# Kernel tuning notes

Hardware: AMD Instinct MI355X
Metric: run time of the kernel (lower is better)

## Reference

```python
import jax, jax.numpy as jnp
import numpy as np

D_MODEL = 256
D_STATE = 16
D_CONV = 4
EXPAND = 2
D_INNER = EXPAND * D_MODEL          # 512
DT_RANK = (D_MODEL + 15) // 16      # 16
B_SZ = 4
L_SEQ = 2048
EPS = 1e-5


def setup_inputs() -> dict:
    key = jax.random.key(0)
    ks = jax.random.split(key, 10)
    s = 0.02
    return {
        "x": jax.random.normal(ks[0], (B_SZ, L_SEQ, D_MODEL), jnp.float32),
        # Mamba params
        "in_proj_w": jax.random.normal(ks[1], (2 * D_INNER, D_MODEL), jnp.float32) * s,
        "conv_w": jax.random.normal(ks[2], (D_INNER, 1, D_CONV), jnp.float32) * s,  # depthwise
        "conv_b": jnp.zeros((D_INNER,), jnp.float32),
        "x_proj_w": jax.random.normal(ks[3], (DT_RANK + 2 * D_STATE, D_INNER), jnp.float32) * s,
        "dt_proj_w": jax.random.normal(ks[4], (D_INNER, DT_RANK), jnp.float32) * s,
        "dt_proj_b": jax.random.uniform(ks[5], (D_INNER,), jnp.float32, -4.0, -2.0),
        "A_log": jnp.log(jnp.broadcast_to(jnp.arange(1, D_STATE + 1, dtype=jnp.float32), (D_INNER, D_STATE))),
        "Dp": jnp.ones((D_INNER,), jnp.float32),
        "out_proj_w": jax.random.normal(ks[6], (D_MODEL, D_INNER), jnp.float32) * s,
        # LayerNorms
        "ln1_g": jnp.ones((D_MODEL,), jnp.float32), "ln1_b": jnp.zeros((D_MODEL,), jnp.float32),
        "ln2_g": jnp.ones((D_MODEL,), jnp.float32), "ln2_b": jnp.zeros((D_MODEL,), jnp.float32),
        # temp_enhance: Conv1d(d_model, d_model, k=3, pad=1, groups=4) + BatchNorm1d (eval buffers)
        "enh_w": jax.random.normal(ks[7], (D_MODEL, D_MODEL // 4, 3), jnp.float32) * s,
        "enh_b": jnp.zeros((D_MODEL,), jnp.float32),
        "bn_g": jnp.ones((D_MODEL,), jnp.float32), "bn_b": jnp.zeros((D_MODEL,), jnp.float32),
        "bn_mean": jnp.zeros((D_MODEL,), jnp.float32), "bn_var": jnp.ones((D_MODEL,), jnp.float32),
    }


def _layernorm(x, g, b):
    m = x.mean(-1, keepdims=True)
    v = ((x - m) ** 2).mean(-1, keepdims=True)
    return (x - m) * jax.lax.rsqrt(v + EPS) * g + b


def _mamba(x, in_proj_w, conv_w, conv_b, x_proj_w, dt_proj_w, dt_proj_b, A_log, Dp, out_proj_w):
    Bb, L, _ = x.shape
    # input projection -> gate z and conv stream
    xz = x @ in_proj_w.T                       # [B, L, 2*d_inner]
    xin, z = jnp.split(xz, 2, axis=-1)
    # causal depthwise conv over time
    xc = jnp.transpose(xin, (0, 2, 1))         # [B, d_inner, L]
    xc = jax.lax.conv_general_dilated(
        xc, conv_w, (1,), [(D_CONV - 1, 0)],
        dimension_numbers=("NCH", "OIH", "NCH"), feature_group_count=D_INNER)
    xc = xc + conv_b[None, :, None]
    xin = jax.nn.silu(jnp.transpose(xc, (0, 2, 1)))   # [B, L, d_inner]
    # input-dependent dt, B, C
    x_dbl = xin @ x_proj_w.T                   # [B, L, dt_rank + 2*d_state]
    dt, Bm, Cm = jnp.split(x_dbl, [DT_RANK, DT_RANK + D_STATE], axis=-1)
    dt = jax.nn.softplus(dt @ dt_proj_w.T + dt_proj_b)   # [B, L, d_inner]
    A = -jnp.exp(A_log)                         # [d_inner, d_state]
    dA = jnp.exp(dt[..., None] * A)             # [B, L, d_inner, d_state]
    dBx = dt[..., None] * Bm[:, :, None, :] * xin[..., None]
    # selective scan: h_t = dA_t * h_{t-1} + dBx_t ; y_t = <h_t, C_t>
    def step(h, inputs):
        a, bx, c = inputs
        h = a * h + bx                          # [B, d_inner, d_state]
        y = jnp.einsum("bds,bs->bd", h, c)
        return h, y
    h0 = jnp.zeros((Bb, D_INNER, D_STATE), x.dtype)
    _, ys = jax.lax.scan(step, h0, (jnp.transpose(dA, (1, 0, 2, 3)),
                                    jnp.transpose(dBx, (1, 0, 2, 3)),
                                    jnp.transpose(Cm, (1, 0, 2))))
    y = jnp.transpose(ys, (1, 0, 2)) + xin * Dp    # skip term D*x
    y = y * jax.nn.silu(z)
    return y @ out_proj_w.T


def reference(x, in_proj_w, conv_w, conv_b, x_proj_w, dt_proj_w, dt_proj_b, A_log, Dp,
              out_proj_w, ln1_g, ln1_b, ln2_g, ln2_b, enh_w, enh_b, bn_g, bn_b, bn_mean, bn_var):
    # dropout is identity in eval mode; BatchNorm uses running stats (eval)
    y = _mamba(x, in_proj_w, conv_w, conv_b, x_proj_w, dt_proj_w, dt_proj_b, A_log, Dp, out_proj_w)
    x1 = _layernorm(y, ln1_g, ln1_b)
    x2 = _layernorm(x + x1, ln2_g, ln2_b)
    # temp_enhance: grouped conv (groups=4) + BN(eval) + GELU on [B, C, L]
    xc = jnp.transpose(x2, (0, 2, 1))
    xc = jax.lax.conv_general_dilated(
        xc, enh_w, (1,), [(1, 1)],
        dimension_numbers=("NCH", "OIH", "NCH"), feature_group_count=4)
    xc = xc + enh_b[None, :, None]
    xc = (xc - bn_mean[None, :, None]) * jax.lax.rsqrt(bn_var[None, :, None] + EPS)
    xc = xc * bn_g[None, :, None] + bn_b[None, :, None]
    xc = jax.nn.gelu(xc, approximate=False)
    return x2 + jnp.transpose(xc, (0, 2, 1))
```

## Files before the change

### kernel.cpp

```cpp
#include <hip/hip_runtime.h>
#include <hip/hip_bf16.h>
#include <math.h>


typedef __attribute__((ext_vector_type(8))) short short8;
typedef __attribute__((ext_vector_type(4))) float f32x4;
typedef unsigned short ushortT;

#define NB    4
#define LSEQ  2048
#define DMODEL 256
#define DINNER 512
#define NTOK  8192
#define NCHUNK 128
#define CT    16
#define ET    16

__device__ __forceinline__ ushortT bf16bits(float f) {
  __hip_bfloat16 h = __float2bfloat16(f);
  return *(ushortT*)&h;
}
__device__ __forceinline__ float b2f(ushortT u) {
  return __bfloat162float(*(const __hip_bfloat16*)&u);
}

__global__ __launch_bounds__(256) void k_prep(
    const float* __restrict__ w_in, const float* __restrict__ w_out,
    const float* __restrict__ A_log, const float* __restrict__ xproj_w,
    const float* __restrict__ enh_w, const float* __restrict__ dtproj_w,
    __hip_bfloat16* __restrict__ wibf, __hip_bfloat16* __restrict__ wobf,
    float* __restrict__ A2L, __hip_bfloat16* __restrict__ xpbf,
    __hip_bfloat16* __restrict__ wenh, __hip_bfloat16* __restrict__ dtwp) {
  int i = blockIdx.x * 256 + threadIdx.x;
  if (i < 1024 * DMODEL)   wibf[i] = __float2bfloat16(w_in[i]);
  if (i < DMODEL * DINNER) wobf[i] = __float2bfloat16(w_out[i]);
  if (i < DINNER * 16)     A2L[i]  = -__expf(A_log[i]) * 1.44269504089f;
  if (i < 64 * 512) {
    int row = i >> 9, col = i & 511;
    xpbf[i] = __float2bfloat16(row < 48 ? xproj_w[row * 512 + col] : 0.0f);
  }
  if (i < 256 * 192) {
    int co = i / 192, k = i - co * 192;
    int kk = k >> 6, ci = k & 63;
    wenh[i] = __float2bfloat16(enh_w[co * 192 + ci * 3 + kk]);
  }
  if (i < 512 * 32) {
    int row = i >> 5, col = i & 31;
    dtwp[i] = __float2bfloat16(col < 16 ? dtproj_w[row * 16 + col] : 0.0f);
  }
}

__global__ __launch_bounds__(256) void gemm_bf(
    const float* __restrict__ A, const ushortT* __restrict__ W,
    __hip_bfloat16* __restrict__ C, int M, int N, int K) {
  __shared__ __align__(16) ushortT Al[64 * 72];
  __shared__ __align__(16) ushortT Wl[64 * 72];
  int tid  = threadIdx.x;
  int mBase = blockIdx.x * 64, nBase = blockIdx.y * 64;
  int wv = tid >> 6, lane = tid & 63, lo = lane & 15, quad = lane >> 4;
  f32x4 acc[4] = {};
  for (int kt = 0; kt < K; kt += 64) {
#pragma unroll
    for (int q = 0; q < 2; ++q) {
      int cid = tid + q * 256;
      int r = cid >> 3, kc = (cid & 7) * 8;
      const float* src = &A[(size_t)(mBase + r) * K + kt + kc];
      float4 f0 = *(const float4*)src;
      float4 f1 = *(const float4*)(src + 4);
      short8 v;
      v[0] = (short)bf16bits(f0.x); v[1] = (short)bf16bits(f0.y);
      v[2] = (short)bf16bits(f0.z); v[3] = (short)bf16bits(f0.w);
      v[4] = (short)bf16bits(f1.x); v[5] = (short)bf16bits(f1.y);
      v[6] = (short)bf16bits(f1.z); v[7] = (short)bf16bits(f1.w);
      *(short8*)&Al[r * 72 + kc] = v;
      *(short8*)&Wl[r * 72 + kc] = *(const short8*)&W[(size_t)(nBase + r) * K + kt + kc];
    }
    __syncthreads();
#pragma unroll
    for (int k0 = 0; k0 < 64; k0 += 32) {
      short8 bfrag = *(short8*)&Wl[(wv * 16 + lo) * 72 + k0 + quad * 8];
#pragma unroll
      for (int mb = 0; mb < 4; ++mb) {
        short8 afrag = *(short8*)&Al[(mb * 16 + lo) * 72 + k0 + quad * 8];
        acc[mb] = __builtin_amdgcn_mfma_f32_16x16x32_bf16(afrag, bfrag, acc[mb], 0, 0, 0);
      }
    }
    __syncthreads();
  }
#pragma unroll
  for (int mb = 0; mb < 4; ++mb)
#pragma unroll
    for (int r = 0; r < 4; ++r) {
      int row = mBase + mb * 16 + quad * 4 + r;
      int col = nBase + wv * 16 + lo;
      C[(size_t)row * N + col] = __float2bfloat16(acc[mb][r]);
    }
}

__device__ __forceinline__ float softplus_fast(float v) {
  return fmaxf(v, 0.0f) + __logf(1.0f + __expf(-fabsf(v)));
}

__device__ __forceinline__ void decay_powers(float a1, float* aa) {
  aa[0] = a1;
#pragma unroll
  for (int s = 1; s < 16; ++s) aa[s] = aa[(s - 1) >> 1] * aa[s >> 1];
}

__device__ __forceinline__ void compute_dt(
    const ushortT* xdt, const ushortT* dtwp_row, float bias, float* dtv) {
  float dtw[16];
#pragma unroll
  for (int s = 0; s < 16; ++s) dtw[s] = b2f(dtwp_row[s]);
#pragma unroll
  for (int t = 0; t < CT; ++t) {
    float acc = 0.f;
#pragma unroll
    for (int s = 0; s < 16; ++s) acc += b2f(xdt[t * 16 + s]) * dtw[s];
    dtv[t] = softplus_fast(acc + bias);
  }
}

__global__ __launch_bounds__(512, 4) void k_convscan(
    const __hip_bfloat16* __restrict__ xzbf, const float* __restrict__ conv_w,
    const float* __restrict__ conv_b, const ushortT* __restrict__ xpbf,
    const ushortT* __restrict__ dtwp, const float* __restrict__ dtb_,
    const float* __restrict__ A2L, __hip_bfloat16* __restrict__ xcbf,
    float* __restrict__ xd, float* __restrict__ Sd, float* __restrict__ Hend) {
  __shared__ __align__(16) ushortT rawx[19 * 520];
  __shared__ __align__(16) ushortT xdt[CT * 16];
  __shared__ __align__(16) float   Bt[CT * 16];
  int tid = threadIdx.x, d = tid;
  int t0 = blockIdx.x * CT, b = blockIdx.y;
  const ushortT* xz = (const ushortT*)xzbf;
  {
    int rloc = tid >> 6;
    int kc = (tid & 63) * 8;
#pragma unroll
    for (int p = 0; p < 3; ++p) {
      int j = p * 8 + rloc;
      if (j < 19) {
        int t = t0 - 3 + j;
        short8 v = {};
        if (t >= 0) v = *(const short8*)&xz[(size_t)(b * LSEQ + t) * 1024 + kc];
        *(short8*)&rawx[j * 520 + kc] = v;
      }
    }
  }
  __syncthreads();
  float4 w4 = *(const float4*)&conv_w[d * 4];
  float cb = conv_b[d];
  float xm3 = b2f(rawx[0 * 520 + d]);
  float xm2 = b2f(rawx[1 * 520 + d]);
  float xm1 = b2f(rawx[2 * 520 + d]);
  float xvr[CT];
  size_t orow = (size_t)(b * LSEQ + t0) * 512 + d;
#pragma unroll
  for (int i = 0; i < CT; ++i) {
    float xt = b2f(rawx[(i + 3) * 520 + d]);
    float acc = cb + w4.x * xm3 + w4.y * xm2 + w4.z * xm1 + w4.w * xt;
    float s = acc / (1.0f + __expf(-acc));
    ushortT sb = bf16bits(s);
    xcbf[orow] = *(__hip_bfloat16*)&sb;
    rawx[i * 520 + d] = sb;
    xvr[i] = b2f(sb);
    orow += 512;
    xm3 = xm2; xm2 = xm1; xm1 = xt;
  }
  __syncthreads();
  int wv = d >> 6, lane = d & 63, lo = lane & 15, quad = lane >> 4;
  int tokb = b * LSEQ + t0;
  if (wv < 4) {
    int nt = wv;
    f32x4 acc = {};
#pragma unroll
    for (int k0 = 0; k0 < 512; k0 += 32) {
      short8 af = *(short8*)&rawx[lo * 520 + k0 + quad * 8];
      short8 bf = *(const short8*)&xpbf[(size_t)(nt * 16 + lo) * 512 + k0 + quad * 8];
      acc = __builtin_amdgcn_mfma_f32_16x16x32_bf16(af, bf, acc, 0, 0, 0);
    }
#pragma unroll
    for (int r = 0; r < 4; ++r)
      xd[(size_t)(tokb + quad * 4 + r) * 64 + nt * 16 + lo] = acc[r];
    if (nt == 0) {
#pragma unroll
      for (int r = 0; r < 4; ++r)
        xdt[(quad * 4 + r) * 16 + lo] = bf16bits(acc[r]);
    }
    if (nt == 1) {
#pragma unroll
      for (int r = 0; r < 4; ++r)
        Bt[(quad * 4 + r) * 16 + lo] = acc[r];
    }
  }
  __syncthreads();
  float dtv[CT];
  compute_dt(xdt, &dtwp[(size_t)d * 32], dtb_[d], dtv);
  float a2l0 = A2L[d * 16];
  float h[16];
#pragma unroll
  for (int s = 0; s < 16; ++s) h[s] = 0.0f;
  float sdt = 0.0f;
#pragma unroll
  for (int t2 = 0; t2 < CT; t2 += 2) {
    float aa[2][16];
    decay_powers(exp2f(dtv[t2 + 0] * a2l0), aa[0]);
    decay_powers(exp2f(dtv[t2 + 1] * a2l0), aa[1]);
#pragma unroll
    for (int j = 0; j < 2; ++j) {
      int tt = t2 + j;
      sdt += dtv[tt];
      float ux = dtv[tt] * xvr[tt];
      const float4* Bp = (const float4*)&Bt[tt * 16];
      float4 B0 = Bp[0], B1 = Bp[1], B2 = Bp[2], B3 = Bp[3];
      float Bv[16] = {B0.x, B0.y, B0.z, B0.w, B1.x, B1.y, B1.z, B1.w,
                      B2.x, B2.y, B2.z, B2.w, B3.x, B3.y, B3.z, B3.w};
#pragma unroll
      for (int s = 0; s < 16; ++s)
        h[s] = aa[j][s] * h[s] + ux * Bv[s];
    }
  }
  int c = blockIdx.x;
  Sd[(size_t)(b * NCHUNK + c) * 512 + d] = sdt;
  size_t basei = ((size_t)(b * NCHUNK + c) * 512 + d) * 16;
#pragma unroll
  for (int q = 0; q < 4; ++q)
    *(float4*)&Hend[basei + q * 4] =
        make_float4(h[q * 4], h[q * 4 + 1], h[q * 4 + 2], h[q * 4 + 3]);
}

__global__ __launch_bounds__(128) void k_scanB(
    const float* __restrict__ Sd, float* __restrict__ Hend,
    const float* __restrict__ A2L) {
  int gid = blockIdx.x * 128 + threadIdx.x;
  int b = gid >> 13, rem = gid & 8191, d = rem >> 4;
  float a2lv = A2L[rem];
  const float* SdB = &Sd[(size_t)b * NCHUNK * 512 + d];
  float* HeB = &Hend[(size_t)b * NCHUNK * 8192 + rem];
  float carry = 0.f;
#pragma unroll 1
  for (int c = 0; c < NCHUNK; c += 8) {
    float sv[8], hv[8], pv[8];
#pragma unroll
    for (int j = 0; j < 8; ++j) sv[j] = SdB[(size_t)(c + j) * 512];
#pragma unroll
    for (int j = 0; j < 8; ++j) hv[j] = HeB[(size_t)(c + j) * 8192];
#pragma unroll
    for (int j = 0; j < 8; ++j) pv[j] = exp2f(a2lv * sv[j]);
#pragma unroll
    for (int j = 0; j < 8; ++j) {
      HeB[(size_t)(c + j) * 8192] = carry;
      carry = pv[j] * carry + hv[j];
    }
  }
}

__global__ __launch_bounds__(512, 4) void k_scanC(
    const __hip_bfloat16* __restrict__ xcbf, const float* __restrict__ xd,
    const ushortT* __restrict__ dtwp, const float* __restrict__ dtb_,
    const float* __restrict__ A2L, const float* __restrict__ Hinit,
    const __hip_bfloat16* __restrict__ xzbf, const float* __restrict__ Dp,
    const ushortT* __restrict__ wobf, float* __restrict__ y2) {
  __shared__ __align__(16) ushortT yt[CT * 520];
  __shared__ __align__(16) ushortT xdt[CT * 16];
  __shared__ __align__(16) float   BCt[CT * 32];
  int tid = threadIdx.x, d = tid;
  int c = blockIdx.x, b = blockIdx.y;
  int tok0 = b * LSEQ + c * CT;
  {
    int t = tid >> 5, cc2 = tid & 31;
    BCt[tid] = xd[(size_t)(tok0 + t) * 64 + 16 + cc2];
  }
  if (tid < 256) {
    int t = tid >> 4, s = tid & 15;
    xdt[t * 16 + s] = bf16bits(xd[(size_t)(tok0 + t) * 64 + s]);
  }
  float a2l0 = A2L[d * 16];
  float h[16];
  size_t basei = ((size_t)(b * NCHUNK + c) * 512 + d) * 16;
#pragma unroll
  for (int q = 0; q < 4; ++q) {
    float4 hv = *(const float4*)&Hinit[basei + q * 4];
    h[q*4] = hv.x; h[q*4+1] = hv.y; h[q*4+2] = hv.z; h[q*4+3] = hv.w;
  }
  float dpv = Dp[d];
  __syncthreads();
  float dtv[CT];
  compute_dt(xdt, &dtwp[(size_t)d * 32], dtb_[d], dtv);
#pragma unroll
  for (int t2 = 0; t2 < CT; t2 += 2) {
    float xv2[2], zv2[2];
#pragma unroll
    for (int j = 0; j < 2; ++j) {
      size_t tok = (size_t)(tok0 + t2 + j);
      xv2[j] = __bfloat162float(xcbf[tok * 512 + d]);
      zv2[j] = __bfloat162float(xzbf[tok * 1024 + 512 + d]);
    }
    float aa[2][16];
    decay_powers(exp2f(dtv[t2 + 0] * a2l0), aa[0]);
    decay_powers(exp2f(dtv[t2 + 1] * a2l0), aa[1]);
#pragma unroll
    for (int j = 0; j < 2; ++j) {
      int t = t2 + j;
      float ux = dtv[t] * xv2[j];
      float y = 0.f;
#pragma unroll
      for (int s = 0; s < 16; ++s) {
        h[s] = aa[j][s] * h[s] + ux * BCt[t * 32 + s];
        y += h[s] * BCt[t * 32 + 16 + s];
      }
      float zv = zv2[j];
      y = (y + xv2[j] * dpv) * (zv / (1.0f + __expf(-zv)));
      yt[t * 520 + d] = bf16bits(y);
    }
  }
  __syncthreads();
  int wv = tid >> 6, lane = tid & 63, lo = lane & 15, quad = lane >> 4;
  f32x4 a0 = {}, a1 = {};
#pragma unroll
  for (int k0 = 0; k0 < 512; k0 += 32) {
    short8 af = *(short8*)&yt[lo * 520 + k0 + quad * 8];
    short8 b0 = *(const short8*)&wobf[(size_t)(wv * 32 + lo) * 512 + k0 + quad * 8];
    short8 b1 = *(const short8*)&wobf[(size_t)(wv * 32 + 16 + lo) * 512 + k0 + quad * 8];
    a0 = __builtin_amdgcn_mfma_f32_16x16x32_bf16(af, b0, a0, 0, 0, 0);
    a1 = __builtin_amdgcn_mfma_f32_16x16x32_bf16(af, b1, a1, 0, 0, 0);
  }
#pragma unroll
  for (int r = 0; r < 4; ++r) {
    int row = tok0 + quad * 4 + r;
    y2[(size_t)row * 256 + wv * 32 + lo]      = a0[r];
    y2[(size_t)row * 256 + wv * 32 + 16 + lo] = a1[r];
  }
}

__global__ __launch_bounds__(256) void k_lnenh(
    const float* __restrict__ y2, const float* __restrict__ x,
    const float* __restrict__ g1, const float* __restrict__ b1,
    const float* __restrict__ g2, const float* __restrict__ b2,
    const ushortT* __restrict__ wenh, const float* __restrict__ enh_b,
    const float* __restrict__ bn_g, const float* __restrict__ bn_b,
    const float* __restrict__ bn_mean, const float* __restrict__ bn_var,
    float* __restrict__ out) {
  __shared__ __align__(16) float   x2f[18 * 264];
  __shared__ __align__(16) ushortT x2h[18 * 264];
  int tid = threadIdx.x, wv = tid >> 6, lane = tid & 63;
  int tb = blockIdx.x, b = blockIdx.y;
  int tbase = tb * ET;
  for (int r = wv; r < 18; r += 4) {
    int t = tbase - 1 + r;
    float4 o = make_float4(0.f, 0.f, 0.f, 0.f);
    if (t >= 0 && t < LSEQ) {
      int tok = b * LSEQ + t;
      float4 v = ((const float4*)&y2[(size_t)tok * DMODEL])[lane];
      float s = v.x + v.y + v.z + v.w;
#pragma unroll
      for (int off = 32; off; off >>= 1) s += __shfl_xor(s, off);
      float m = s * (1.0f / DMODEL);
      float4 dv = make_float4(v.x - m, v.y - m, v.z - m, v.w - m);
      float q = dv.x*dv.x + dv.y*dv.y + dv.z*dv.z + dv.w*dv.w;
#pragma unroll
      for (int off = 32; off; off >>= 1) q += __shfl_xor(q, off);
      float rs = rsqrtf(q * (1.0f / DMODEL) + 1e-5f);
      float4 gg = ((const float4*)g1)[lane], bb = ((const float4*)b1)[lane];
      float4 xv = ((const float4*)&x[(size_t)tok * DMODEL])[lane];
      float4 tt;
      tt.x = xv.x + dv.x * rs * gg.x + bb.x;
      tt.y = xv.y + dv.y * rs * gg.y + bb.y;
      tt.z = xv.z + dv.z * rs * gg.z + bb.z;
      tt.w = xv.w + dv.w * rs * gg.w + bb.w;
      float s2 = tt.x + tt.y + tt.z + tt.w;
#pragma unroll
      for (int off = 32; off; off >>= 1) s2 += __shfl_xor(s2, off);
      float m2 = s2 * (1.0f / DMODEL);
      float4 d2 = make_float4(tt.x - m2, tt.y - m2, tt.z - m2, tt.w - m2);
      float q2 = d2.x*d2.x + d2.y*d2.y + d2.z*d2.z + d2.w*d2.w;
#pragma unroll
      for (int off = 32; off; off >>= 1) q2 += __shfl_xor(q2, off);
      float rs2 = rsqrtf(q2 * (1.0f / DMODEL) + 1e-5f);
      float4 g2v = ((const float4*)g2)[lane], b2v = ((const float4*)b2)[lane];
      o.x = d2.x * rs2 * g2v.x + b2v.x;
      o.y = d2.y * rs2 * g2v.y + b2v.y;
      o.z = d2.z * rs2 * g2v.z + b2v.z;
      o.w = d2.w * rs2 * g2v.w + b2v.w;
    }
    *(float4*)&x2f[r * 264 + lane * 4] = o;
    ushortT p[4];
    p[0] = bf16bits(o.x); p[1] = bf16bits(o.y);
    p[2] = bf16bits(o.z); p[3] = bf16bits(o.w);
    *(uint2*)&x2h[r * 264 + lane * 4] = *(uint2*)p;
  }
  __syncthreads();
  int g = wv, lo = lane & 15, quad = lane >> 4;
  short8 af[6];
#pragma unroll
  for (int ks = 0; ks < 6; ++ks) {
    int kk = ks >> 1, cb = (ks & 1) * 32;
    af[ks] = *(short8*)&x2h[(lo + kk) * 264 + g * 64 + cb + quad * 8];
  }
  f32x4 acc[4] = {};
#pragma unroll
  for (int nt = 0; nt < 4; ++nt) {
    int co = g * 64 + nt * 16 + lo;
#pragma unroll
    for (int ks = 0; ks < 6; ++ks) {
      short8 bf = *(const short8*)&wenh[(size_t)co * 192 + ks * 32 + quad * 8];
      acc[nt] = __builtin_amdgcn_mfma_f32_16x16x32_bf16(af[ks], bf, acc[nt], 0, 0, 0);
    }
  }
#pragma unroll
  for (int nt = 0; nt < 4; ++nt) {
    int co = g * 64 + nt * 16 + lo;
    float scale = bn_g[co] * rsqrtf(bn_var[co] + 1e-5f);
    float shift = bn_b[co] - bn_mean[co] * scale;
    float ebv = enh_b[co];
#pragma unroll
    for (int r = 0; r < 4; ++r) {
      int m = quad * 4 + r;
      float v = (acc[nt][r] + ebv) * scale + shift;
      float ge = 0.5f * v * (1.0f + erff(v * 0.70710678118f));
      out[(size_t)(b * LSEQ + tbase + m) * DMODEL + co] = x2f[(m + 1) * 264 + co] + ge;
    }
  }
}

extern "C" void kernel_launch(void* const* d_in, const int* in_sizes, int n_in,
                              void* d_out, int out_size, void* d_ws, size_t ws_size,
                              hipStream_t stream) {
  const float* x        = (const float*)d_in[0];
  const float* in_w     = (const float*)d_in[1];
  const float* conv_w   = (const float*)d_in[2];
  const float* conv_b   = (const float*)d_in[3];
  const float* xproj_w  = (const float*)d_in[4];
  const float* dtproj_w = (const float*)d_in[5];
  const float* dtproj_b = (const float*)d_in[6];
  const float* A_log    = (const float*)d_in[7];
  const float* Dp       = (const float*)d_in[8];
  const float* out_w    = (const float*)d_in[9];
  const float* ln1_g    = (const float*)d_in[10];
  const float* ln1_b    = (const float*)d_in[11];
  const float* ln2_g    = (const float*)d_in[12];
  const float* ln2_b    = (const float*)d_in[13];
  const float* enh_w    = (const float*)d_in[14];
  const float* enh_b    = (const float*)d_in[15];
  const float* bn_g     = (const float*)d_in[16];
  const float* bn_b     = (const float*)d_in[17];
  const float* bn_mean  = (const float*)d_in[18];
  const float* bn_var   = (const float*)d_in[19];
  float* out = (float*)d_out;

  char* ws = (char*)d_ws;
  size_t off = 0;
  auto alloc = [&](size_t bytes) { char* p = ws + off; off += (bytes + 255) & ~(size_t)255; return p; };
  __hip_bfloat16* xzbf = (__hip_bfloat16*)alloc((size_t)NTOK * 1024 * 2);
  __hip_bfloat16* xcbf = (__hip_bfloat16*)alloc((size_t)NTOK * 512 * 2);
  float*          xd   = (float*)alloc((size_t)NTOK * 64 * 4);
  float*          A2L  = (float*)alloc((size_t)DINNER * 16 * 4);
  __hip_bfloat16* wibf = (__hip_bfloat16*)alloc((size_t)1024 * DMODEL * 2);
  __hip_bfloat16* wobf = (__hip_bfloat16*)alloc((size_t)DMODEL * DINNER * 2);
  __hip_bfloat16* xpbf = (__hip_bfloat16*)alloc((size_t)64 * 512 * 2);
  __hip_bfloat16* wenh = (__hip_bfloat16*)alloc((size_t)256 * 192 * 2);
  __hip_bfloat16* dtwp = (__hip_bfloat16*)alloc((size_t)512 * 32 * 2);
  float*          Sd   = (float*)alloc((size_t)NB * NCHUNK * 512 * 4);
  float*          He   = (float*)alloc((size_t)NB * NCHUNK * 512 * 16 * 4);
  float*          y2   = (float*)alloc((size_t)NTOK * DMODEL * 4);
  (void)ws_size; (void)in_sizes; (void)n_in; (void)out_size;

  k_prep<<<1024, 256, 0, stream>>>(in_w, out_w, A_log, xproj_w, enh_w, dtproj_w,
                                   wibf, wobf, A2L, xpbf, wenh, dtwp);
  gemm_bf<<<dim3(128, 16), 256, 0, stream>>>(x, (const ushortT*)wibf,
                                             xzbf, NTOK, 1024, DMODEL);
  k_convscan<<<dim3(NCHUNK, 4), 512, 0, stream>>>(xzbf, conv_w, conv_b,
                                              (const ushortT*)xpbf, (const ushortT*)dtwp,
                                              dtproj_b, A2L, xcbf, xd, Sd, He);
  k_scanB<<<256, 128, 0, stream>>>(Sd, He, A2L);
  k_scanC<<<dim3(NCHUNK, 4), 512, 0, stream>>>(xcbf, xd, (const ushortT*)dtwp,
                                               dtproj_b, A2L, He, xzbf, Dp,
                                               (const ushortT*)wobf, y2);
  k_lnenh<<<dim3(LSEQ / ET, 4), 256, 0, stream>>>(y2, x, ln1_g, ln1_b, ln2_g, ln2_b,
                                                  (const ushortT*)wenh, enh_b,
                                                  bn_g, bn_b, bn_mean, bn_var, out);
}
```

Measured before the change: 189.2 us.

## Compute dt projection with MFMA and shuffles; transpose chunk state layout

Replaces the per-thread scalar 16x16 dt projection in the conv-scan and output-scan kernels with a bf16 MFMA per wave, padding the dt input tile to K=32 with zeros and redistributing results via lane shuffles. It also changes the Hend/Hinit chunk-state layout from [d][s] to [s][d], so per-thread stores and loads and the k_scanB accesses are coalesced across d. The aim is to cut the FMA and LDS-read cost of the dt projection and to reduce strided global traffic on the state arrays. The cost is extra shuffles, an MFMA per wave, and a bit more shared-memory zeroing.

```diff
diff --git a/kernel.cpp b/kernel.cpp
--- a/kernel.cpp
+++ b/kernel.cpp
@@ -107,17 +107,29 @@
   for (int s = 1; s < 16; ++s) aa[s] = aa[(s - 1) >> 1] * aa[s >> 1];
 }
 
-__device__ __forceinline__ void compute_dt(
-    const ushortT* xdt, const ushortT* dtwp_row, float bias, float* dtv) {
-  float dtw[16];
-#pragma unroll
-  for (int s = 0; s < 16; ++s) dtw[s] = b2f(dtwp_row[s]);
+__device__ __forceinline__ void dt_mfma_shfl(
+    const ushortT* xdt, const ushortT* __restrict__ dtwp,
+    int d, int wv, int lo, int quad, float biasd, float* dtv) {
+  short8 af2 = *(short8*)&xdt[lo * 32 + quad * 8];
+  f32x4 a2v[4];
+#pragma unroll
+  for (int i = 0; i < 4; ++i) {
+    int ntc = wv * 4 + i;
+    short8 bf2 = *(const short8*)&dtwp[(size_t)(ntc * 16 + lo) * 32 + quad * 8];
+    a2v[i] = __builtin_amdgcn_mfma_f32_16x16x32_bf16(af2, bf2, (f32x4){}, 0, 0, 0);
+  }
+  int i_need = (d >> 4) & 3;
+  int bsrc = d & 15;
 #pragma unroll
   for (int t = 0; t < CT; ++t) {
-    float acc = 0.f;
-#pragma unroll
-    for (int s = 0; s < 16; ++s) acc += b2f(xdt[t * 16 + s]) * dtw[s];
-    dtv[t] = softplus_fast(acc + bias);
+    int src = (t >> 2) * 16 + bsrc;
+    float v = 0.f;
+#pragma unroll
+    for (int ii = 0; ii < 4; ++ii) {
+      float sv = __shfl(a2v[ii][t & 3], src);
+      if (ii == i_need) v = sv;
+    }
+    dtv[t] = softplus_fast(v + biasd);
   }
 }
 
@@ -128,11 +140,12 @@
     const float* __restrict__ A2L, __hip_bfloat16* __restrict__ xcbf,
     float* __restrict__ xd, float* __restrict__ Sd, float* __restrict__ Hend) {
   __shared__ __align__(16) ushortT rawx[19 * 520];
-  __shared__ __align__(16) ushortT xdt[CT * 16];
+  __shared__ __align__(16) ushortT xdt[16 * 32];
   __shared__ __align__(16) float   Bt[CT * 16];
   int tid = threadIdx.x, d = tid;
   int t0 = blockIdx.x * CT, b = blockIdx.y;
   const ushortT* xz = (const ushortT*)xzbf;
+  if (tid < 256) ((unsigned int*)xdt)[tid] = 0u;
   {
     int rloc = tid >> 6;
     int kc = (tid & 63) * 8;
@@ -185,7 +198,7 @@
     if (nt == 0) {
 #pragma unroll
       for (int r = 0; r < 4; ++r)
-        xdt[(quad * 4 + r) * 16 + lo] = bf16bits(acc[r]);
+        xdt[(quad * 4 + r) * 32 + lo] = bf16bits(acc[r]);
     }
     if (nt == 1) {
 #pragma unroll
@@ -195,7 +208,7 @@
   }
   __syncthreads();
   float dtv[CT];
-  compute_dt(xdt, &dtwp[(size_t)d * 32], dtb_[d], dtv);
+  dt_mfma_shfl(xdt, dtwp, d, wv, lo, quad, dtb_[d], dtv);
   float a2l0 = A2L[d * 16];
   float h[16];
 #pragma unroll
@@ -222,19 +235,19 @@
   }
   int c = blockIdx.x;
   Sd[(size_t)(b * NCHUNK + c) * 512 + d] = sdt;
-  size_t basei = ((size_t)(b * NCHUNK + c) * 512 + d) * 16;
-#pragma unroll
-  for (int q = 0; q < 4; ++q)
-    *(float4*)&Hend[basei + q * 4] =
-        make_float4(h[q * 4], h[q * 4 + 1], h[q * 4 + 2], h[q * 4 + 3]);
+  size_t hbase = (size_t)(b * NCHUNK + c) * 8192 + d;
+#pragma unroll
+  for (int s = 0; s < 16; ++s)
+    Hend[hbase + (size_t)s * 512] = h[s];
 }
 
 __global__ __launch_bounds__(128) void k_scanB(
     const float* __restrict__ Sd, float* __restrict__ Hend,
     const float* __restrict__ A2L) {
   int gid = blockIdx.x * 128 + threadIdx.x;
-  int b = gid >> 13, rem = gid & 8191, d = rem >> 4;
-  float a2lv = A2L[rem];
+  int b = gid >> 13, rem = gid & 8191;
+  int d = rem & 511, s = rem >> 9;
+  float a2lv = A2L[d * 16 + s];
   const float* SdB = &Sd[(size_t)b * NCHUNK * 512 + d];
   float* HeB = &Hend[(size_t)b * NCHUNK * 8192 + rem];
   float carry = 0.f;
@@ -262,7 +275,7 @@
     const __hip_bfloat16* __restrict__ xzbf, const float* __restrict__ Dp,
     const ushortT* __restrict__ wobf, float* __restrict__ y2) {
   __shared__ __align__(16) ushortT yt[CT * 520];
-  __shared__ __align__(16) ushortT xdt[CT * 16];
+  __shared__ __align__(16) ushortT xdt[CT * 32];
   __shared__ __align__(16) float   BCt[CT * 32];
   int tid = threadIdx.x, d = tid;
   int c = blockIdx.x, b = blockIdx.y;
@@ -273,20 +286,19 @@
   }
   if (tid < 256) {
     int t = tid >> 4, s = tid & 15;
-    xdt[t * 16 + s] = bf16bits(xd[(size_t)(tok0 + t) * 64 + s]);
+    xdt[t * 32 + s] = bf16bits(xd[(size_t)(tok0 + t) * 64 + s]);
+    xdt[t * 32 + 16 + s] = 0;
   }
   float a2l0 = A2L[d * 16];
   float h[16];
-  size_t basei = ((size_t)(b * NCHUNK + c) * 512 + d) * 16;
-#pragma unroll
-  for (int q = 0; q < 4; ++q) {
-    float4 hv = *(const float4*)&Hinit[basei + q * 4];
-    h[q*4] = hv.x; h[q*4+1] = hv.y; h[q*4+2] = hv.z; h[q*4+3] = hv.w;
-  }
+  size_t hbase = (size_t)(b * NCHUNK + c) * 8192 + d;
+#pragma unroll
+  for (int s = 0; s < 16; ++s) h[s] = Hinit[hbase + (size_t)s * 512];
   float dpv = Dp[d];
   __syncthreads();
+  int wv = tid >> 6, lane = tid & 63, lo = lane & 15, quad = lane >> 4;
   float dtv[CT];
-  compute_dt(xdt, &dtwp[(size_t)d * 32], dtb_[d], dtv);
+  dt_mfma_shfl(xdt, dtwp, d, wv, lo, quad, dtb_[d], dtv);
 #pragma unroll
   for (int t2 = 0; t2 < CT; t2 += 2) {
     float xv2[2], zv2[2];
@@ -315,7 +327,6 @@
     }
   }
   __syncthreads();
-  int wv = tid >> 6, lane = tid & 63, lo = lane & 15, quad = lane >> 4;
   f32x4 a0 = {}, a1 = {};
 #pragma unroll
   for (int k0 = 0; k0 < 512; k0 += 32) {
```

Measured after the change: 183.3 us. -3.1%, faster.
